# Optimization experiments

Measured on AMD Instinct MI355X. Metric: run time of the kernel, lower is better.

## Reference

```python
import jax, jax.numpy as jnp
import numpy as np

B, N_IN, N_OUT, H = 64, 5023, 5023, 256
EPS = 1e-12  # matches torch F.normalize default eps


def setup_inputs() -> dict:
    key = jax.random.key(0)
    k1, k2, k3, k4 = jax.random.split(key, 4)
    return {
        "x": jax.random.normal(k1, (B, N_IN, 3), dtype=jnp.float32),
        "key_w": jax.random.normal(k2, (N_IN, H), dtype=jnp.float32) * (1.0 / np.sqrt(H)),
        "query_w": jax.random.normal(k3, (H, N_OUT), dtype=jnp.float32) * (1.0 / np.sqrt(H)),
        "value_w": jax.random.normal(k4, (3, 3), dtype=jnp.float32),
    }


def reference(x, key_w, query_w, value_w):
    # v = nn.Linear(3,3,bias=False)(x): x @ W^T        [B, N_in, 3]
    v = jnp.einsum("bnd,ed->bne", x, value_w)
    # score = (key @ query) / sqrt(hidden_dim)          [N_in, N_out]
    scale = jnp.asarray(key_w.shape[-1], x.dtype) ** 0.5
    score = jnp.matmul(key_w, query_w) / scale
    # L1 normalization along dim=1 (F.normalize p=1)
    l1 = jnp.sum(jnp.abs(score), axis=1, keepdims=True)
    score = score / jnp.maximum(l1, EPS)
    # y = score.T @ v (dropout is identity in eval / p=0) [B, N_out, 3]
    return jnp.einsum("io,bid->bod", score, v)
```

## Files before the change

### kernel.cpp

```cpp
#include <hip/hip_runtime.h>
#include <hip/hip_bf16.h>

#define N_IN   5023
#define B_SZ   64
#define H_DIM  256
#define NPAD   5120
#define NBD    192
#define SPLITZ 20
#define OUT_ELEMS (B_SZ * N_IN * 3)

typedef short bf16x8 __attribute__((ext_vector_type(8)));
typedef float f32x4  __attribute__((ext_vector_type(4)));

__device__ inline void async_copy16(const void* g, void* l) {
    __builtin_amdgcn_global_load_lds(
        (const __attribute__((address_space(1))) unsigned int*)g,
        (__attribute__((address_space(3))) unsigned int*)l,
        16, 0, 0);
}

__global__ void conv_key_all(const float* __restrict__ kw, short* __restrict__ keyb,
                             short* __restrict__ keyT, float* __restrict__ l1) {
    __shared__ float tile[32][33];
    const int hb = blockIdx.x * 32;
    const int ib = blockIdx.y * 32;
    const int tx = threadIdx.x;
    const int ty = threadIdx.y;
    __hip_bfloat16* kb = (__hip_bfloat16*)keyb;
    __hip_bfloat16* kt = (__hip_bfloat16*)keyT;
    for (int j = 0; j < 32; j += 8) {
        int i = ib + ty + j;
        int h = hb + tx;
        float v = (i < N_IN) ? kw[(size_t)i * H_DIM + h] : 0.0f;
        tile[ty + j][tx] = v;
        kb[(size_t)i * H_DIM + h] = __float2bfloat16(v);
    }
    __syncthreads();
    for (int j = 0; j < 32; j += 8) {
        int h = hb + ty + j;
        int i = ib + tx;
        kt[(size_t)h * NPAD + i] = __float2bfloat16(tile[tx][ty + j]);
    }
    if (blockIdx.x == 0 && ty == 0) l1[ib + tx] = 0.0f;
}

__global__ void conv_qt(const float* __restrict__ qw, short* __restrict__ qtb) {
    __shared__ float tile[32][33];
    const int hb = blockIdx.x * 32;
    const int ob = blockIdx.y * 32;
    const int tx = threadIdx.x;
    const int ty = threadIdx.y;
    for (int j = 0; j < 32; j += 8) {
        int h = hb + ty + j;
        int o = ob + tx;
        tile[ty + j][tx] = (o < N_IN) ? qw[(size_t)h * N_IN + o] * 0.0625f : 0.0f;
    }
    __syncthreads();
    __hip_bfloat16* qt = (__hip_bfloat16*)qtb;
    for (int j = 0; j < 32; j += 8) {
        int o = ob + ty + j;
        int h = hb + tx;
        qt[(size_t)o * H_DIM + h] = __float2bfloat16(tile[tx][ty + j]);
    }
}

#define HALF_ELEMS (NPAD * H_DIM / 2)
__global__ void conv_fp8(const short* __restrict__ qtb, const short* __restrict__ keyb,
                         unsigned short* __restrict__ q8, unsigned short* __restrict__ k8) {
    int idx = blockIdx.x * 256 + threadIdx.x;
    bool isK = idx >= HALF_ELEMS;
    int p = isK ? idx - HALF_ELEMS : idx;
    const __hip_bfloat16* src = (const __hip_bfloat16*)(isK ? keyb : qtb);
    float a = __bfloat162float(src[2 * p]);
    float b = __bfloat162float(src[2 * p + 1]);
    if (!isK) { a *= 16.0f; b *= 16.0f; }
    int packed = __builtin_amdgcn_cvt_pk_fp8_f32(a, b, 0, false);
    (isK ? k8 : q8)[p] = (unsigned short)(packed & 0xFFFF);
}

__launch_bounds__(256)
__global__ void gemm_l1(const unsigned char* __restrict__ q8,
                        const unsigned char* __restrict__ k8,
                        float* __restrict__ l1) {
    __shared__ unsigned char As8[128 * 128];
    __shared__ unsigned char Bs8[128 * 128];
    const int bm = blockIdx.x, bn = blockIdx.y;
    const int tid = threadIdx.x, lane = tid & 63, wid = tid >> 6;
    const int wave_m = wid >> 1, wave_n = wid & 1;
    const int r = lane >> 3;
    const int s = lane & 7;
    const int quad = lane >> 4, cit = lane & 15;
    const int xk = cit & 7;

    f32x4 acc[4][4];
    const f32x4 zf = {0.f, 0.f, 0.f, 0.f};
    for (int a = 0; a < 4; ++a)
        for (int b = 0; b < 4; ++b) acc[a][b] = zf;

    for (int kb = 0; kb < H_DIM; kb += 128) {
        __syncthreads();
        const int koff = kb + ((s ^ r) << 4);
        for (int c = 0; c < 4; ++c) {
            int q = wid * 4 + c;
            int row = q * 8 + r;
            async_copy16(q8 + (size_t)(bm * 128 + row) * H_DIM + koff, As8 + q * 1024);
            async_copy16(k8 + (size_t)(bn * 128 + row) * H_DIM + koff, Bs8 + q * 1024);
        }
        __syncthreads();
        for (int ki = 0; ki < 4; ++ki) {
            int g = ki * 2 + (quad >> 1);
            int lo8 = (quad & 1) << 3;
            int slot = ((g ^ xk) << 4) + lo8;
            long af[4], bf[4];
            for (int t = 0; t < 4; ++t) {
                int am = wave_m * 64 + t * 16 + cit;
                af[t] = *(const long*)(As8 + am * 128 + slot);
                int bn_ = wave_n * 64 + t * 16 + cit;
                bf[t] = *(const long*)(Bs8 + bn_ * 128 + slot);
            }
            for (int tm = 0; tm < 4; ++tm)
                for (int tn = 0; tn < 4; ++tn)
                    acc[tm][tn] = __builtin_amdgcn_mfma_f32_16x16x32_fp8_fp8(
                        af[tm], bf[tn], acc[tm][tn], 0, 0, 0);
        }
    }

    for (int tn = 0; tn < 4; ++tn) {
        int ig = bn * 128 + wave_n * 64 + tn * 16 + cit;
        float p = 0.0f;
        for (int tm = 0; tm < 4; ++tm) {
            f32x4 c = acc[tm][tn];
            p += fabsf(c.x) + fabsf(c.y) + fabsf(c.z) + fabsf(c.w);
        }
        p += __shfl_xor(p, 16);
        p += __shfl_xor(p, 32);
        if (quad == 0) atomicAdd(&l1[ig], p);
    }
}

__global__ void build_vmat(const float* __restrict__ x, const float* __restrict__ vw,
                           const float* __restrict__ l1, short* __restrict__ vmatT) {
    int idx = blockIdx.x * 256 + threadIdx.x;
    if (idx >= B_SZ * NPAD) return;
    int b = idx / NPAD, i = idx % NPAD;
    __hip_bfloat16* vt = (__hip_bfloat16*)vmatT;
    if (i < N_IN) {
        const float* xp = x + ((size_t)b * N_IN + i) * 3;
        float x0 = xp[0], x1 = xp[1], x2 = xp[2];
        float r = 1.0f / fmaxf(l1[i] * 0.0625f, 1e-12f);
        for (int e = 0; e < 3; ++e) {
            float v = x0 * vw[e * 3 + 0] + x1 * vw[e * 3 + 1] + x2 * vw[e * 3 + 2];
            vt[(size_t)(b * 3 + e) * NPAD + i] = __float2bfloat16(v * r);
        }
    } else {
        for (int e = 0; e < 3; ++e)
            vt[(size_t)(b * 3 + e) * NPAD + i] = __float2bfloat16(0.0f);
    }
}

__launch_bounds__(256)
__global__ void gemm3(const short* __restrict__ vmatT, const short* __restrict__ keyT,
                      float* __restrict__ part2) {
    __shared__ short As[192 * 64];
    __shared__ short Bs[64 * 64];
    const int bh = blockIdx.x;
    const int z  = blockIdx.y;
    const int tid = threadIdx.x, lane = tid & 63, wid = tid >> 6;
    const int wave_m = wid >> 1, wave_n = wid & 1;
    const int srow = lane >> 3, scol = (lane & 7) * 8;
    const int quad = lane >> 4, cit = lane & 15;

    f32x4 acc[6][2];
    const f32x4 zf = {0.f, 0.f, 0.f, 0.f};
    for (int a = 0; a < 6; ++a)
        for (int b = 0; b < 2; ++b) acc[a][b] = zf;

    const int kbeg = z * (NPAD / SPLITZ);
    for (int kb = kbeg; kb < kbeg + NPAD / SPLITZ; kb += 64) {
        __syncthreads();
        for (int c = 0; c < 6; ++c) {
            int q = wid * 6 + c;
            int row = q * 8 + srow;
            async_copy16(vmatT + (size_t)row * NPAD + kb + scol, As + q * 512);
        }
        for (int c = 0; c < 2; ++c) {
            int q = wid * 2 + c;
            int row = q * 8 + srow;
            async_copy16(keyT + (size_t)(bh * 64 + row) * NPAD + kb + scol, Bs + q * 512);
        }
        __syncthreads();
        for (int kk = 0; kk < 64; kk += 32) {
            bf16x8 af[6], bf[2];
            int ko = kk + quad * 8;
            for (int t = 0; t < 6; ++t)
                af[t] = *(const bf16x8*)(As + (wave_m * 96 + t * 16 + cit) * 64 + ko);
            for (int t = 0; t < 2; ++t)
                bf[t] = *(const bf16x8*)(Bs + (wave_n * 32 + t * 16 + cit) * 64 + ko);
            for (int tm = 0; tm < 6; ++tm)
                for (int tn = 0; tn < 2; ++tn)
                    acc[tm][tn] = __builtin_amdgcn_mfma_f32_16x16x32_bf16(
                        af[tm], bf[tn], acc[tm][tn], 0, 0, 0);
        }
    }

    float* pz = part2 + (size_t)z * (NBD * H_DIM);
    for (int tn = 0; tn < 2; ++tn) {
        int h = bh * 64 + wave_n * 32 + tn * 16 + cit;
        for (int tm = 0; tm < 6; ++tm) {
            int bd0 = wave_m * 96 + tm * 16 + quad * 4;
            f32x4 c = acc[tm][tn];
            for (int r = 0; r < 4; ++r)
                pz[(size_t)(bd0 + r) * H_DIM + h] = c[r];
        }
    }
}

__global__ void reduce_T(const float* __restrict__ part2, short* __restrict__ T) {
    int idx = blockIdx.x * 256 + threadIdx.x;
    float s = 0.0f;
    for (int z = 0; z < SPLITZ; ++z)
        s += part2[(size_t)z * (NBD * H_DIM) + idx];
    ((__hip_bfloat16*)T)[idx] = __float2bfloat16(s);
}

#define CS_PITCH 196
__launch_bounds__(256)
__global__ void gemm4(const short* __restrict__ qt, const short* __restrict__ T,
                      float* __restrict__ out) {
    __shared__ char smem[64 * CS_PITCH * 4];
    short* As = (short*)smem;
    short* Bs = As + 64 * 64;
    const int bm = blockIdx.x;
    const int tid = threadIdx.x, lane = tid & 63, wid = tid >> 6;
    const int wave_m = wid >> 1, wave_n = wid & 1;
    const int srow = lane >> 3, scol = (lane & 7) * 8;
    const int quad = lane >> 4, cit = lane & 15;

    f32x4 acc[2][6];
    const f32x4 zf = {0.f, 0.f, 0.f, 0.f};
    for (int a = 0; a < 2; ++a)
        for (int b = 0; b < 6; ++b) acc[a][b] = zf;

    for (int kb = 0; kb < H_DIM; kb += 64) {
        __syncthreads();
        for (int c = 0; c < 2; ++c) {
            int q = wid * 2 + c;
            int row = q * 8 + srow;
            async_copy16(qt + (size_t)(bm * 64 + row) * H_DIM + kb + scol, As + q * 512);
        }
        for (int c = 0; c < 6; ++c) {
            int q = wid * 6 + c;
            int row = q * 8 + srow;
            async_copy16(T + (size_t)row * H_DIM + kb + scol, Bs + q * 512);
        }
        __syncthreads();
        for (int kk = 0; kk < 64; kk += 32) {
            bf16x8 af[2], bf[6];
            int ko = kk + quad * 8;
            for (int t = 0; t < 2; ++t)
                af[t] = *(const bf16x8*)(As + (wave_m * 32 + t * 16 + cit) * 64 + ko);
            for (int t = 0; t < 6; ++t)
                bf[t] = *(const bf16x8*)(Bs + (wave_n * 96 + t * 16 + cit) * 64 + ko);
            for (int tm = 0; tm < 2; ++tm)
                for (int tn = 0; tn < 6; ++tn)
                    acc[tm][tn] = __builtin_amdgcn_mfma_f32_16x16x32_bf16(
                        af[tm], bf[tn], acc[tm][tn], 0, 0, 0);
        }
    }

    __syncthreads();
    float* cs = (float*)smem;
    for (int tn = 0; tn < 6; ++tn) {
        int bd = wave_n * 96 + tn * 16 + cit;
        for (int tm = 0; tm < 2; ++tm) {
            int o0 = wave_m * 32 + tm * 16 + quad * 4;
            f32x4 c = acc[tm][tn];
            for (int r = 0; r < 4; ++r)
                cs[(o0 + r) * CS_PITCH + bd] = c[r];
        }
    }
    __syncthreads();
    for (int it = 0; it < 48; ++it) {
        int flat = it * 256 + tid;
        int b = flat / NBD;
        int w = flat - b * NBD;
        int o_l = w / 3, d = w - o_l * 3;
        int og = bm * 64 + o_l;
        if (og < N_IN)
            out[(size_t)b * (N_IN * 3) + (size_t)og * 3 + d] =
                cs[o_l * CS_PITCH + b * 3 + d];
    }
}

extern "C" void kernel_launch(void* const* d_in, const int* in_sizes, int n_in,
                              void* d_out, int out_size, void* d_ws, size_t ws_size,
                              hipStream_t stream) {
    const float* x  = (const float*)d_in[0];
    const float* kw = (const float*)d_in[1];
    const float* qw = (const float*)d_in[2];
    const float* vw = (const float*)d_in[3];
    float* out = (float*)d_out;

    char* w = (char*)d_ws;
    short* keyb  = (short*)(w + 0);
    short* qtb   = (short*)(w + 2621440);
    short* keyT  = (short*)(w + 5242880);
    short* vmatT = (short*)(w + 7864320);
    float* l1    = (float*)(w + 9830400);
    float* part2 = (float*)(w + 9850880);
    short* T     = (short*)(w + 13783040);
    unsigned short* q8 = (unsigned short*)(w + 13881344);
    unsigned short* k8 = (unsigned short*)(w + 15192064);

    conv_key_all<<<dim3(H_DIM / 32, NPAD / 32), dim3(32, 8), 0, stream>>>(kw, keyb, keyT, l1);
    conv_qt<<<dim3(H_DIM / 32, NPAD / 32), dim3(32, 8), 0, stream>>>(qw, qtb);
    conv_fp8<<<(2 * HALF_ELEMS) / 256, 256, 0, stream>>>(qtb, keyb, q8, k8);
    gemm_l1<<<dim3(NPAD / 128, NPAD / 128), 256, 0, stream>>>(
        (const unsigned char*)q8, (const unsigned char*)k8, l1);
    build_vmat<<<(B_SZ * NPAD) / 256, 256, 0, stream>>>(x, vw, l1, vmatT);
    gemm3<<<dim3(H_DIM / 64, SPLITZ), 256, 0, stream>>>(vmatT, keyT, part2);
    reduce_T<<<(NBD * H_DIM) / 256, 256, 0, stream>>>(part2, T);
    gemm4<<<NPAD / 64, 256, 0, stream>>>(qtb, T, out);
}
```

Before: 111.6 us.

## Fuse conversion kernels, fold vmat build into gemm3, retile gemm4 and swizzle LDS

Merges the key and query conversion kernels and the separate fp8 conversion pass into one launch that writes fp8 directly from fp32. Removes build_vmat by computing the normalized value tile inside gemm3 from x and l1, with SPLITZ raised so each block handles one 64-wide K slice. gemm4 moves to 32-row tiles for more blocks, and XOR swizzling is added to the LDS layouts to cut bank conflicts. Launches and intermediate global traffic go down, at the cost of more partial sums for reduce_T and recomputing the value tile in every h-block.

New measurement: 107.8 us (median of 2 runs). 3.4% less time.

```diff
diff --git a/kernel.cpp b/kernel.cpp
--- a/kernel.cpp
+++ b/kernel.cpp
@@ -6,7 +6,7 @@
 #define H_DIM  256
 #define NPAD   5120
 #define NBD    192
-#define SPLITZ 20
+#define SPLITZ 80
 #define OUT_ELEMS (B_SZ * N_IN * 3)
 
 typedef short bf16x8 __attribute__((ext_vector_type(8)));
@@ -19,63 +19,52 @@
         16, 0, 0);
 }
 
-__global__ void conv_key_all(const float* __restrict__ kw, short* __restrict__ keyb,
-                             short* __restrict__ keyT, float* __restrict__ l1) {
+__device__ inline unsigned char to_fp8(float v) {
+    int p = __builtin_amdgcn_cvt_pk_fp8_f32(v, 0.0f, 0, false);
+    return (unsigned char)(p & 0xFF);
+}
+
+__global__ void conv_all(const float* __restrict__ kw, const float* __restrict__ qw,
+                         unsigned char* __restrict__ k8, short* __restrict__ keyT,
+                         unsigned char* __restrict__ q8, short* __restrict__ qtb,
+                         float* __restrict__ l1) {
     __shared__ float tile[32][33];
     const int hb = blockIdx.x * 32;
-    const int ib = blockIdx.y * 32;
+    const int nb = blockIdx.y * 32;
     const int tx = threadIdx.x;
     const int ty = threadIdx.y;
-    __hip_bfloat16* kb = (__hip_bfloat16*)keyb;
-    __hip_bfloat16* kt = (__hip_bfloat16*)keyT;
-    for (int j = 0; j < 32; j += 8) {
-        int i = ib + ty + j;
-        int h = hb + tx;
-        float v = (i < N_IN) ? kw[(size_t)i * H_DIM + h] : 0.0f;
-        tile[ty + j][tx] = v;
-        kb[(size_t)i * H_DIM + h] = __float2bfloat16(v);
-    }
-    __syncthreads();
-    for (int j = 0; j < 32; j += 8) {
-        int h = hb + ty + j;
-        int i = ib + tx;
-        kt[(size_t)h * NPAD + i] = __float2bfloat16(tile[tx][ty + j]);
-    }
-    if (blockIdx.x == 0 && ty == 0) l1[ib + tx] = 0.0f;
-}
-
-__global__ void conv_qt(const float* __restrict__ qw, short* __restrict__ qtb) {
-    __shared__ float tile[32][33];
-    const int hb = blockIdx.x * 32;
-    const int ob = blockIdx.y * 32;
-    const int tx = threadIdx.x;
-    const int ty = threadIdx.y;
-    for (int j = 0; j < 32; j += 8) {
-        int h = hb + ty + j;
-        int o = ob + tx;
-        tile[ty + j][tx] = (o < N_IN) ? qw[(size_t)h * N_IN + o] * 0.0625f : 0.0f;
-    }
-    __syncthreads();
-    __hip_bfloat16* qt = (__hip_bfloat16*)qtb;
-    for (int j = 0; j < 32; j += 8) {
-        int o = ob + ty + j;
-        int h = hb + tx;
-        qt[(size_t)o * H_DIM + h] = __float2bfloat16(tile[tx][ty + j]);
-    }
-}
-
-#define HALF_ELEMS (NPAD * H_DIM / 2)
-__global__ void conv_fp8(const short* __restrict__ qtb, const short* __restrict__ keyb,
-                         unsigned short* __restrict__ q8, unsigned short* __restrict__ k8) {
-    int idx = blockIdx.x * 256 + threadIdx.x;
-    bool isK = idx >= HALF_ELEMS;
-    int p = isK ? idx - HALF_ELEMS : idx;
-    const __hip_bfloat16* src = (const __hip_bfloat16*)(isK ? keyb : qtb);
-    float a = __bfloat162float(src[2 * p]);
-    float b = __bfloat162float(src[2 * p + 1]);
-    if (!isK) { a *= 16.0f; b *= 16.0f; }
-    int packed = __builtin_amdgcn_cvt_pk_fp8_f32(a, b, 0, false);
-    (isK ? k8 : q8)[p] = (unsigned short)(packed & 0xFFFF);
+    if (blockIdx.z == 0) {
+        for (int j = 0; j < 32; j += 8) {
+            int i = nb + ty + j;
+            int h = hb + tx;
+            float v = (i < N_IN) ? kw[(size_t)i * H_DIM + h] : 0.0f;
+            tile[ty + j][tx] = v;
+            k8[(size_t)i * H_DIM + h] = to_fp8(v);
+        }
+        __syncthreads();
+        __hip_bfloat16* kt = (__hip_bfloat16*)keyT;
+        for (int j = 0; j < 32; j += 8) {
+            int h = hb + ty + j;
+            int i = nb + tx;
+            kt[(size_t)h * NPAD + i] = __float2bfloat16(tile[tx][ty + j]);
+        }
+        if (blockIdx.x == 0 && ty == 0) l1[nb + tx] = 0.0f;
+    } else {
+        for (int j = 0; j < 32; j += 8) {
+            int h = hb + ty + j;
+            int o = nb + tx;
+            tile[ty + j][tx] = (o < N_IN) ? qw[(size_t)h * N_IN + o] : 0.0f;
+        }
+        __syncthreads();
+        __hip_bfloat16* qt = (__hip_bfloat16*)qtb;
+        for (int j = 0; j < 32; j += 8) {
+            int o = nb + ty + j;
+            int h = hb + tx;
+            float v = tile[tx][ty + j];
+            qt[(size_t)o * H_DIM + h] = __float2bfloat16(v * 0.0625f);
+            q8[(size_t)o * H_DIM + h] = to_fp8(v);
+        }
+    }
 }
 
 __launch_bounds__(256)
@@ -138,69 +127,71 @@
     }
 }
 
-__global__ void build_vmat(const float* __restrict__ x, const float* __restrict__ vw,
-                           const float* __restrict__ l1, short* __restrict__ vmatT) {
-    int idx = blockIdx.x * 256 + threadIdx.x;
-    if (idx >= B_SZ * NPAD) return;
-    int b = idx / NPAD, i = idx % NPAD;
-    __hip_bfloat16* vt = (__hip_bfloat16*)vmatT;
-    if (i < N_IN) {
-        const float* xp = x + ((size_t)b * N_IN + i) * 3;
-        float x0 = xp[0], x1 = xp[1], x2 = xp[2];
-        float r = 1.0f / fmaxf(l1[i] * 0.0625f, 1e-12f);
-        for (int e = 0; e < 3; ++e) {
-            float v = x0 * vw[e * 3 + 0] + x1 * vw[e * 3 + 1] + x2 * vw[e * 3 + 2];
-            vt[(size_t)(b * 3 + e) * NPAD + i] = __float2bfloat16(v * r);
-        }
-    } else {
-        for (int e = 0; e < 3; ++e)
-            vt[(size_t)(b * 3 + e) * NPAD + i] = __float2bfloat16(0.0f);
-    }
-}
-
+#define AP 72
 __launch_bounds__(256)
-__global__ void gemm3(const short* __restrict__ vmatT, const short* __restrict__ keyT,
-                      float* __restrict__ part2) {
-    __shared__ short As[192 * 64];
+__global__ void gemm3_f(const float* __restrict__ x, const float* __restrict__ vw,
+                        const float* __restrict__ l1, const short* __restrict__ keyT,
+                        float* __restrict__ part2) {
+    __shared__ short As[NBD * AP];
     __shared__ short Bs[64 * 64];
     const int bh = blockIdx.x;
     const int z  = blockIdx.y;
     const int tid = threadIdx.x, lane = tid & 63, wid = tid >> 6;
     const int wave_m = wid >> 1, wave_n = wid & 1;
-    const int srow = lane >> 3, scol = (lane & 7) * 8;
+    const int rr = lane >> 3, ss = lane & 7;
     const int quad = lane >> 4, cit = lane & 15;
+
+    {
+        const int i_loc = tid & 63;
+        const int grp   = tid >> 6;
+        const int i = z * 64 + i_loc;
+        const bool ok = (i < N_IN);
+        float rcp = 0.0f;
+        if (ok) rcp = 1.0f / fmaxf(l1[i] * 0.0625f, 1e-12f);
+        float w00 = vw[0], w01 = vw[1], w02 = vw[2];
+        float w10 = vw[3], w11 = vw[4], w12 = vw[5];
+        float w20 = vw[6], w21 = vw[7], w22 = vw[8];
+        __hip_bfloat16* as = (__hip_bfloat16*)As;
+        for (int bo = 0; bo < 16; ++bo) {
+            int b = grp * 16 + bo;
+            float x0 = 0.f, x1 = 0.f, x2 = 0.f;
+            if (ok) {
+                const float* xp = x + ((size_t)b * N_IN + i) * 3;
+                x0 = xp[0]; x1 = xp[1]; x2 = xp[2];
+            }
+            as[(b * 3 + 0) * AP + i_loc] = __float2bfloat16((x0 * w00 + x1 * w01 + x2 * w02) * rcp);
+            as[(b * 3 + 1) * AP + i_loc] = __float2bfloat16((x0 * w10 + x1 * w11 + x2 * w12) * rcp);
+            as[(b * 3 + 2) * AP + i_loc] = __float2bfloat16((x0 * w20 + x1 * w21 + x2 * w22) * rcp);
+        }
+    }
+    for (int c = 0; c < 2; ++c) {
+        int q = wid * 2 + c;
+        int row = q * 8 + rr;
+        int koff = z * 64 + ((ss ^ (rr & 7)) << 3);
+        async_copy16(keyT + (size_t)(bh * 64 + row) * NPAD + koff, Bs + q * 512);
+    }
+    __syncthreads();
 
     f32x4 acc[6][2];
     const f32x4 zf = {0.f, 0.f, 0.f, 0.f};
     for (int a = 0; a < 6; ++a)
         for (int b = 0; b < 2; ++b) acc[a][b] = zf;
 
-    const int kbeg = z * (NPAD / SPLITZ);
-    for (int kb = kbeg; kb < kbeg + NPAD / SPLITZ; kb += 64) {
-        __syncthreads();
-        for (int c = 0; c < 6; ++c) {
-            int q = wid * 6 + c;
-            int row = q * 8 + srow;
-            async_copy16(vmatT + (size_t)row * NPAD + kb + scol, As + q * 512);
-        }
-        for (int c = 0; c < 2; ++c) {
-            int q = wid * 2 + c;
-            int row = q * 8 + srow;
-            async_copy16(keyT + (size_t)(bh * 64 + row) * NPAD + kb + scol, Bs + q * 512);
-        }
-        __syncthreads();
-        for (int kk = 0; kk < 64; kk += 32) {
-            bf16x8 af[6], bf[2];
-            int ko = kk + quad * 8;
-            for (int t = 0; t < 6; ++t)
-                af[t] = *(const bf16x8*)(As + (wave_m * 96 + t * 16 + cit) * 64 + ko);
-            for (int t = 0; t < 2; ++t)
-                bf[t] = *(const bf16x8*)(Bs + (wave_n * 32 + t * 16 + cit) * 64 + ko);
-            for (int tm = 0; tm < 6; ++tm)
-                for (int tn = 0; tn < 2; ++tn)
-                    acc[tm][tn] = __builtin_amdgcn_mfma_f32_16x16x32_bf16(
-                        af[tm], bf[tn], acc[tm][tn], 0, 0, 0);
-        }
+    for (int kk = 0; kk < 64; kk += 32) {
+        bf16x8 af[6], bf[2];
+        int g = (kk >> 3) + quad;
+        for (int t = 0; t < 6; ++t) {
+            int row = wave_m * 96 + t * 16 + cit;
+            af[t] = *(const bf16x8*)(As + row * AP + kk + quad * 8);
+        }
+        for (int t = 0; t < 2; ++t) {
+            int row = wave_n * 32 + t * 16 + cit;
+            bf[t] = *(const bf16x8*)(Bs + row * 64 + ((g ^ (cit & 7)) << 3));
+        }
+        for (int tm = 0; tm < 6; ++tm)
+            for (int tn = 0; tn < 2; ++tn)
+                acc[tm][tn] = __builtin_amdgcn_mfma_f32_16x16x32_bf16(
+                    af[tm], bf[tn], acc[tm][tn], 0, 0, 0);
     }
 
     float* pz = part2 + (size_t)z * (NBD * H_DIM);
@@ -209,8 +200,8 @@
         for (int tm = 0; tm < 6; ++tm) {
             int bd0 = wave_m * 96 + tm * 16 + quad * 4;
             f32x4 c = acc[tm][tn];
-            for (int r = 0; r < 4; ++r)
-                pz[(size_t)(bd0 + r) * H_DIM + h] = c[r];
+            for (int r2 = 0; r2 < 4; ++r2)
+                pz[(size_t)(bd0 + r2) * H_DIM + h] = c[r2];
         }
     }
 }
@@ -227,44 +218,47 @@
 __launch_bounds__(256)
 __global__ void gemm4(const short* __restrict__ qt, const short* __restrict__ T,
                       float* __restrict__ out) {
-    __shared__ char smem[64 * CS_PITCH * 4];
+    __shared__ __align__(16) char smem[28672];
     short* As = (short*)smem;
-    short* Bs = As + 64 * 64;
+    short* Bs = (short*)(smem + 4096);
     const int bm = blockIdx.x;
     const int tid = threadIdx.x, lane = tid & 63, wid = tid >> 6;
     const int wave_m = wid >> 1, wave_n = wid & 1;
-    const int srow = lane >> 3, scol = (lane & 7) * 8;
+    const int rr = lane >> 3, ss = lane & 7;
     const int quad = lane >> 4, cit = lane & 15;
 
-    f32x4 acc[2][6];
+    f32x4 acc[6];
     const f32x4 zf = {0.f, 0.f, 0.f, 0.f};
-    for (int a = 0; a < 2; ++a)
-        for (int b = 0; b < 6; ++b) acc[a][b] = zf;
+    for (int b = 0; b < 6; ++b) acc[b] = zf;
 
     for (int kb = 0; kb < H_DIM; kb += 64) {
         __syncthreads();
-        for (int c = 0; c < 2; ++c) {
-            int q = wid * 2 + c;
-            int row = q * 8 + srow;
-            async_copy16(qt + (size_t)(bm * 64 + row) * H_DIM + kb + scol, As + q * 512);
+        const int koff = kb + ((ss ^ (rr & 7)) << 3);
+        {
+            int row = wid * 8 + rr;
+            async_copy16(qt + (size_t)(bm * 32 + row) * H_DIM + koff, As + wid * 512);
         }
         for (int c = 0; c < 6; ++c) {
             int q = wid * 6 + c;
-            int row = q * 8 + srow;
-            async_copy16(T + (size_t)row * H_DIM + kb + scol, Bs + q * 512);
+            int row = q * 8 + rr;
+            async_copy16(T + (size_t)row * H_DIM + koff, Bs + q * 512);
         }
         __syncthreads();
         for (int kk = 0; kk < 64; kk += 32) {
-            bf16x8 af[2], bf[6];
-            int ko = kk + quad * 8;
-            for (int t = 0; t < 2; ++t)
-                af[t] = *(const bf16x8*)(As + (wave_m * 32 + t * 16 + cit) * 64 + ko);
-            for (int t = 0; t < 6; ++t)
-                bf[t] = *(const bf16x8*)(Bs + (wave_n * 96 + t * 16 + cit) * 64 + ko);
-            for (int tm = 0; tm < 2; ++tm)
-                for (int tn = 0; tn < 6; ++tn)
-                    acc[tm][tn] = __builtin_amdgcn_mfma_f32_16x16x32_bf16(
-                        af[tm], bf[tn], acc[tm][tn], 0, 0, 0);
+            bf16x8 af, bf[6];
+            int g = (kk >> 3) + quad;
+            int slot = (g ^ (cit & 7)) << 3;
+            {
+                int row = wave_m * 16 + cit;
+                af = *(const bf16x8*)(As + row * 64 + slot);
+            }
+            for (int t = 0; t < 6; ++t) {
+                int row = wave_n * 96 + t * 16 + cit;
+                bf[t] = *(const bf16x8*)(Bs + row * 64 + slot);
+            }
+            for (int tn = 0; tn < 6; ++tn)
+                acc[tn] = __builtin_amdgcn_mfma_f32_16x16x32_bf16(
+                    af, bf[tn], acc[tn], 0, 0, 0);
         }
     }
 
@@ -272,20 +266,18 @@
     float* cs = (float*)smem;
     for (int tn = 0; tn < 6; ++tn) {
         int bd = wave_n * 96 + tn * 16 + cit;
-        for (int tm = 0; tm < 2; ++tm) {
-            int o0 = wave_m * 32 + tm * 16 + quad * 4;
-            f32x4 c = acc[tm][tn];
-            for (int r = 0; r < 4; ++r)
-                cs[(o0 + r) * CS_PITCH + bd] = c[r];
-        }
+        int o0 = wave_m * 16 + quad * 4;
+        f32x4 c = acc[tn];
+        for (int r2 = 0; r2 < 4; ++r2)
+            cs[(o0 + r2) * CS_PITCH + bd] = c[r2];
     }
     __syncthreads();
-    for (int it = 0; it < 48; ++it) {
+    for (int it = 0; it < 24; ++it) {
         int flat = it * 256 + tid;
-        int b = flat / NBD;
-        int w = flat - b * NBD;
+        int b = flat / 96;
+        int w = flat - b * 96;
         int o_l = w / 3, d = w - o_l * 3;
-        int og = bm * 64 + o_l;
+        int og = bm * 32 + o_l;
         if (og < N_IN)
             out[(size_t)b * (N_IN * 3) + (size_t)og * 3 + d] =
                 cs[o_l * CS_PITCH + b * 3 + d];
@@ -302,23 +294,18 @@
     float* out = (float*)d_out;
 
     char* w = (char*)d_ws;
-    short* keyb  = (short*)(w + 0);
-    short* qtb   = (short*)(w + 2621440);
-    short* keyT  = (short*)(w + 5242880);
-    short* vmatT = (short*)(w + 7864320);
-    float* l1    = (float*)(w + 9830400);
-    float* part2 = (float*)(w + 9850880);
-    short* T     = (short*)(w + 13783040);
-    unsigned short* q8 = (unsigned short*)(w + 13881344);
-    unsigned short* k8 = (unsigned short*)(w + 15192064);
-
-    conv_key_all<<<dim3(H_DIM / 32, NPAD / 32), dim3(32, 8), 0, stream>>>(kw, keyb, keyT, l1);
-    conv_qt<<<dim3(H_DIM / 32, NPAD / 32), dim3(32, 8), 0, stream>>>(qw, qtb);
-    conv_fp8<<<(2 * HALF_ELEMS) / 256, 256, 0, stream>>>(qtb, keyb, q8, k8);
-    gemm_l1<<<dim3(NPAD / 128, NPAD / 128), 256, 0, stream>>>(
-        (const unsigned char*)q8, (const unsigned char*)k8, l1);
-    build_vmat<<<(B_SZ * NPAD) / 256, 256, 0, stream>>>(x, vw, l1, vmatT);
-    gemm3<<<dim3(H_DIM / 64, SPLITZ), 256, 0, stream>>>(vmatT, keyT, part2);
+    short* qtb  = (short*)(w + 0);
+    short* keyT = (short*)(w + 2621440);
+    unsigned char* q8 = (unsigned char*)(w + 5242880);
+    unsigned char* k8 = (unsigned char*)(w + 6553600);
+    float* l1    = (float*)(w + 7864320);
+    float* part2 = (float*)(w + 7884800);
+    short* T     = (short*)(w + 23613440);
+
+    conv_all<<<dim3(H_DIM / 32, NPAD / 32, 2), dim3(32, 8), 0, stream>>>(
+        kw, qw, k8, keyT, q8, qtb, l1);
+    gemm_l1<<<dim3(NPAD / 128, NPAD / 128), 256, 0, stream>>>(q8, k8, l1);
+    gemm3_f<<<dim3(H_DIM / 64, SPLITZ), 256, 0, stream>>>(x, vw, l1, keyT, part2);
     reduce_T<<<(NBD * H_DIM) / 256, 256, 0, stream>>>(part2, T);
-    gemm4<<<NPAD / 64, 256, 0, stream>>>(qtb, T, out);
-}
+    gemm4<<<NPAD / 32, 256, 0, stream>>>(qtb, T, out);
+}
```
